# Kernel tuning notes

Measured on AMD Instinct MI355X. Metric: run time of the kernel, lower is better.

## Reference

```python
import jax, jax.numpy as jnp
import numpy as np
from jax import lax

LBDA = 0.5   # soft-min temperature from OTAM_cum_dist_v2 default
EPS = 0.01   # cos_sim epsilon


def otam_cum_dist(dists, lbda=LBDA):
    """Soft-DTW-style OTAM DP. dists: [nq, ns, L, S] -> [nq, ns].
    Faithful to OTAM_cum_dist_v2: pad last dim by (1,1) with zeros, then run the
    row-wise recurrence. Soft-min computed via stable logsumexp (same math as
    -lbda*log(sum exp(-x/lbda)))."""
    nq, ns, L, S = dists.shape
    d = jnp.pad(dists, ((0, 0), (0, 0), (0, 0), (1, 1)))  # [nq, ns, L, W], W=S+2
    W = S + 2
    # Row 0: cum[0, m] = cum[0, m-1] + d[0, m], cum[0, 0] = 0
    row0 = jnp.concatenate(
        [jnp.zeros((nq, ns, 1), d.dtype), jnp.cumsum(d[:, :, 0, 1:], axis=-1)], axis=-1)
    if L == 1:
        return row0[..., -1]

    m_idx = jnp.arange(1, W)
    include_up = (m_idx == 1) | (m_idx == W - 1)  # only first/last cols use cum[l-1, m]
    INF = jnp.asarray(jnp.inf, d.dtype)

    def row_step(prev_row, d_row):
        # prev_row, d_row: [nq, ns, W]
        xs = (
            jnp.moveaxis(d_row[:, :, 1:], -1, 0),        # d[l, m],       [W-1, nq, ns]
            jnp.moveaxis(prev_row[:, :, :-1], -1, 0),    # cum[l-1, m-1]
            jnp.moveaxis(prev_row[:, :, 1:], -1, 0),     # cum[l-1, m]
            include_up,
        )

        def col_step(cur_left, x):
            d_m, p_diag, p_up, inc = x
            up = jnp.where(inc, p_up, INF)               # masked term -> exp(-inf)=0
            terms = jnp.stack([p_diag, cur_left, up])    # [3, nq, ns]
            new = d_m - lbda * jax.nn.logsumexp(-terms / lbda, axis=0)
            return new, new

        _, cols = lax.scan(col_step, jnp.zeros((nq, ns), d.dtype), xs)
        row = jnp.concatenate(
            [jnp.zeros((nq, ns, 1), d.dtype), jnp.moveaxis(cols, 0, -1)], axis=-1)
        return row, None

    d_rows = jnp.moveaxis(d[:, :, 1:, :], 2, 0)          # [L-1, nq, ns, W]
    final_row, _ = lax.scan(row_step, row0, d_rows)
    return final_row[..., -1]


def reference(support_features, query_features):
    """OTAM meta-logits (cum_dist_g = -otam_distance) of DSN_TEMPORAL.
    support_features: [n_classes, L, D] class prototypes; query_features: [nq, L, D]."""
    nq, Lq, D = query_features.shape
    ns, Ls, _ = support_features.shape
    q = query_features.reshape(nq * Lq, D)
    s = support_features.reshape(ns * Ls, D)
    # cos_sim with epsilon in denominator (faithful to cos_sim())
    num = q @ s.T
    den = (jnp.linalg.norm(q, axis=-1)[:, None]
           * jnp.linalg.norm(s, axis=-1)[None, :] + EPS)
    frame_dists = 1.0 - num / den                         # [nq*L, ns*S]
    dists = frame_dists.reshape(nq, Lq, ns, Ls).transpose(0, 2, 1, 3)  # [nq, ns, L, S]
    cum = otam_cum_dist(dists) + otam_cum_dist(dists.transpose(0, 1, 3, 2))
    return -cum                                           # meta_logits [nq, ns]


def setup_inputs() -> dict:
    key = jax.random.key(0)
    k1, k2 = jax.random.split(key)
    return {
        "support_features": jax.random.normal(k1, (64, 8, 576), dtype=jnp.float32),
        "query_features": jax.random.normal(k2, (2048, 8, 576), dtype=jnp.float32),
    }
```

## Files before the change

### kernel.cpp

```cpp
#include <hip/hip_runtime.h>

#define D_K 576
#define NSLAB 18
#define LBDA_INV 2.0f
#define HALF_LBDA 0.5f
#define EPS 0.01f
#define DSTRIDE 136
#define DT_STRIDE 72
#define POOL_USHORTS 17920

typedef __attribute__((ext_vector_type(8))) short short8;
typedef __attribute__((ext_vector_type(4))) float f32x4;

__device__ inline unsigned cvt_pk_bf16(float lo, float hi) {
    unsigned r;
    asm("v_cvt_pk_bf16_f32 %0, %1, %2" : "=v"(r) : "v"(lo), "v"(hi));
    return r;
}

__device__ inline float softmin2(float a, float b) {
    float mn = fminf(a, b), mx = fmaxf(a, b);
    return mn - HALF_LBDA * __logf(1.f + __expf(LBDA_INV * (mn - mx)));
}
__device__ inline float softmin3(float a, float b, float c) {
    float mn = fminf(fminf(a, b), c);
    float mx = fmaxf(fmaxf(a, b), c);
    float md = __builtin_amdgcn_fmed3f(a, b, c);
    float s = 1.f + __expf(LBDA_INV * (mn - md)) + __expf(LBDA_INV * (mn - mx));
    return mn - HALF_LBDA * __logf(s);
}

template <int STRIDE>
__device__ float otam_dp_rows(const unsigned short* base) {
    float x[8], prev[10], cur[10];
    auto load_row = [&](int l) {
        uint4 v = *(const uint4*)(base + l * STRIDE);
        x[0] = __uint_as_float(v.x << 16);
        x[1] = __uint_as_float(v.x & 0xFFFF0000u);
        x[2] = __uint_as_float(v.y << 16);
        x[3] = __uint_as_float(v.y & 0xFFFF0000u);
        x[4] = __uint_as_float(v.z << 16);
        x[5] = __uint_as_float(v.z & 0xFFFF0000u);
        x[6] = __uint_as_float(v.w << 16);
        x[7] = __uint_as_float(v.w & 0xFFFF0000u);
    };
    load_row(0);
    prev[0] = 0.f;
#pragma unroll
    for (int m = 1; m <= 8; ++m) prev[m] = prev[m - 1] + x[m - 1];
    prev[9] = prev[8];
#pragma unroll
    for (int l = 1; l < 8; ++l) {
        load_row(l);
        cur[0] = 0.f;
        cur[1] = x[0] + softmin3(prev[0], 0.f, prev[1]);
#pragma unroll
        for (int m = 2; m <= 8; ++m)
            cur[m] = x[m - 1] + softmin2(prev[m - 1], cur[m - 1]);
        cur[9] = softmin3(prev[8], cur[8], prev[9]);
#pragma unroll
        for (int m = 0; m < 10; ++m) prev[m] = cur[m];
    }
    return prev[9];
}

__global__ __launch_bounds__(256, 4) void fused_kernel(
        const float* __restrict__ sup, const float* __restrict__ qry,
        float* __restrict__ out) {
    __shared__ __align__(16) unsigned short pool[POOL_USHORTS];
    __shared__ float qn_l[64], sn_l[128];
    unsigned short* const Bs0 = pool;
    unsigned short* const Bs1 = pool + 4096;
    unsigned short* const Ds  = pool;
    unsigned short* const DsT = pool + 8704;

    const int t = threadIdx.x;
    const int b = blockIdx.x;
    const int xcd = b & 7, s2 = b >> 3;
    const int sblk = s2 >> 5;
    const int qh = xcd * 32 + (s2 & 31);

    const float* qsrc = qry + (size_t)qh * 64 * D_K;
    const float* ssrc = sup + (size_t)sblk * 128 * D_K;

    const int rr = t >> 3;
    const int cc = t & 7;
    const int c_in = cc >> 1, half = cc & 1;

    const int lane = t & 63;
    const int wave = t >> 6;
    const int wm = wave >> 1, wn = wave & 1;
    const int col16 = lane & 15, quad = lane >> 4;

    f32x4 acc[2][4];
#pragma unroll
    for (int i = 0; i < 2; ++i)
#pragma unroll
        for (int j = 0; j < 4; ++j) acc[i][j] = (f32x4){0.f, 0.f, 0.f, 0.f};

    int agoff[2];
#pragma unroll
    for (int mt = 0; mt < 2; ++mt)
        agoff[mt] = (wm * 32 + mt * 16 + col16) * D_K + quad * 8;

    int boff[4], woff[4];
#pragma unroll
    for (int nt = 0; nt < 4; ++nt) {
        int n = wn * 64 + nt * 16 + col16;
        boff[nt] = (quad * 128 + (n ^ (quad << 1))) * 8;
    }
#pragma unroll
    for (int j = 0; j < 4; ++j)
        woff[j] = (c_in * 128 + ((j * 32 + rr) ^ (c_in << 1))) * 8 + half * 4;

    float ssA[2] = {0.f, 0.f}, ssB[4] = {0.f, 0.f, 0.f, 0.f};
    float4 vb[4];

    auto stage_load = [&](int sl) {
        const int off = sl * 32 + cc * 4;
#pragma unroll
        for (int j = 0; j < 4; ++j)
            vb[j] = *(const float4*)(ssrc + (size_t)(j * 32 + rr) * D_K + off);
    };
    auto stage_write = [&](unsigned short* __restrict__ B) {
#pragma unroll
        for (int j = 0; j < 4; ++j) {
            ssB[j] += vb[j].x * vb[j].x + vb[j].y * vb[j].y +
                      vb[j].z * vb[j].z + vb[j].w * vb[j].w;
            uint2 u;
            u.x = cvt_pk_bf16(vb[j].x, vb[j].y);
            u.y = cvt_pk_bf16(vb[j].z, vb[j].w);
            *(uint2*)(&B[woff[j]]) = u;
        }
    };
    auto compute = [&](int sl, const unsigned short* __restrict__ B) {
        float4 a0[2], a1[2];
#pragma unroll
        for (int mt = 0; mt < 2; ++mt) {
            const float* ap = qsrc + agoff[mt] + sl * 32;
            a0[mt] = *(const float4*)(ap);
            a1[mt] = *(const float4*)(ap + 4);
        }
        short8 bq[4];
#pragma unroll
        for (int nt = 0; nt < 4; ++nt) bq[nt] = *(const short8*)(&B[boff[nt]]);
        short8 af[2];
#pragma unroll
        for (int mt = 0; mt < 2; ++mt) {
            ssA[mt] += a0[mt].x * a0[mt].x + a0[mt].y * a0[mt].y +
                       a0[mt].z * a0[mt].z + a0[mt].w * a0[mt].w +
                       a1[mt].x * a1[mt].x + a1[mt].y * a1[mt].y +
                       a1[mt].z * a1[mt].z + a1[mt].w * a1[mt].w;
            uint4 u;
            u.x = cvt_pk_bf16(a0[mt].x, a0[mt].y);
            u.y = cvt_pk_bf16(a0[mt].z, a0[mt].w);
            u.z = cvt_pk_bf16(a1[mt].x, a1[mt].y);
            u.w = cvt_pk_bf16(a1[mt].z, a1[mt].w);
            af[mt] = *(short8*)&u;
        }
#pragma unroll
        for (int mt = 0; mt < 2; ++mt)
#pragma unroll
            for (int nt = 0; nt < 4; ++nt)
                acc[mt][nt] = __builtin_amdgcn_mfma_f32_16x16x32_bf16(
                    af[mt], bq[nt], acc[mt][nt], 0, 0, 0);
    };

    stage_load(0);
    stage_write(Bs0);
    __syncthreads();

#pragma unroll 1
    for (int sp = 0; sp < 9; ++sp) {
        stage_load(2 * sp + 1);
        compute(2 * sp, Bs0);
        stage_write(Bs1);
        __syncthreads();
        if (sp < 8) stage_load(2 * sp + 2);
        compute(2 * sp + 1, Bs1);
        if (sp < 8) stage_write(Bs0);
        __syncthreads();
    }

#pragma unroll
    for (int mt = 0; mt < 2; ++mt) {
        float a = ssA[mt];
        a += __shfl_down(a, 32);
        a += __shfl_down(a, 16);
        if (wn == 0 && lane < 16) qn_l[wm * 32 + mt * 16 + lane] = sqrtf(a);
    }
#pragma unroll
    for (int j = 0; j < 4; ++j) {
        float s = ssB[j];
        s += __shfl_down(s, 4); s += __shfl_down(s, 2); s += __shfl_down(s, 1);
        if ((t & 7) == 0) sn_l[j * 32 + rr] = sqrtf(s);
    }
    __syncthreads();

#pragma unroll
    for (int mt = 0; mt < 2; ++mt) {
        const int m = wm * 32 + mt * 16 + quad * 4;
        float q0 = qn_l[m], q1 = qn_l[m + 1], q2 = qn_l[m + 2], q3 = qn_l[m + 3];
#pragma unroll
        for (int nt = 0; nt < 4; ++nt) {
            const int n = wn * 64 + nt * 16 + col16;
            float sv = sn_l[n];
            float d0 = 1.f - acc[mt][nt][0] * __builtin_amdgcn_rcpf(q0 * sv + EPS);
            float d1 = 1.f - acc[mt][nt][1] * __builtin_amdgcn_rcpf(q1 * sv + EPS);
            float d2 = 1.f - acc[mt][nt][2] * __builtin_amdgcn_rcpf(q2 * sv + EPS);
            float d3 = 1.f - acc[mt][nt][3] * __builtin_amdgcn_rcpf(q3 * sv + EPS);
            uint2 u;
            u.x = cvt_pk_bf16(d0, d1);
            u.y = cvt_pk_bf16(d2, d3);
            *(uint2*)(&DsT[n * DT_STRIDE + m]) = u;
            Ds[(m + 0) * DSTRIDE + n] = (unsigned short)(u.x);
            Ds[(m + 1) * DSTRIDE + n] = (unsigned short)(u.x >> 16);
            Ds[(m + 2) * DSTRIDE + n] = (unsigned short)(u.y);
            Ds[(m + 3) * DSTRIDE + n] = (unsigned short)(u.y >> 16);
        }
    }
    __syncthreads();

    const int p = t & 127, ql = p >> 4, sj = p & 15;
    float r;
    if (t < 128) {
        r = otam_dp_rows<DSTRIDE>(Ds + (ql * 8) * DSTRIDE + sj * 8);
    } else {
        r = otam_dp_rows<DT_STRIDE>(DsT + (sj * 8) * DT_STRIDE + ql * 8);
        sn_l[p] = r;
    }
    __syncthreads();
    if (t < 128) {
        int qg = qh * 8 + ql, sg = sblk * 16 + sj;
        out[qg * 64 + sg] = -(r + sn_l[p]);
    }
}

extern "C" void kernel_launch(void* const* d_in, const int* in_sizes, int n_in,
                              void* d_out, int out_size, void* d_ws, size_t ws_size,
                              hipStream_t stream) {
    const float* sup = (const float*)d_in[0];
    const float* qry = (const float*)d_in[1];
    float* out = (float*)d_out;
    (void)d_ws; (void)ws_size;
    fused_kernel<<<dim3(1024), dim3(256), 0, stream>>>(sup, qry, out);
}
```

Baseline: 127.1 us.

## Load support B fragments directly from global memory, dropping LDS staging

```diff
diff --git a/kernel.cpp b/kernel.cpp
--- a/kernel.cpp
+++ b/kernel.cpp
@@ -69,8 +69,6 @@
         float* __restrict__ out) {
     __shared__ __align__(16) unsigned short pool[POOL_USHORTS];
     __shared__ float qn_l[64], sn_l[128];
-    unsigned short* const Bs0 = pool;
-    unsigned short* const Bs1 = pool + 4096;
     unsigned short* const Ds  = pool;
     unsigned short* const DsT = pool + 8704;
 
@@ -83,10 +81,6 @@
     const float* qsrc = qry + (size_t)qh * 64 * D_K;
     const float* ssrc = sup + (size_t)sblk * 128 * D_K;
 
-    const int rr = t >> 3;
-    const int cc = t & 7;
-    const int c_in = cc >> 1, half = cc & 1;
-
     const int lane = t & 63;
     const int wave = t >> 6;
     const int wm = wave >> 1, wn = wave & 1;
@@ -98,52 +92,32 @@
 #pragma unroll
         for (int j = 0; j < 4; ++j) acc[i][j] = (f32x4){0.f, 0.f, 0.f, 0.f};
 
-    int agoff[2];
+    int agoff[2], bgoff[4];
 #pragma unroll
     for (int mt = 0; mt < 2; ++mt)
         agoff[mt] = (wm * 32 + mt * 16 + col16) * D_K + quad * 8;
-
-    int boff[4], woff[4];
-#pragma unroll
-    for (int nt = 0; nt < 4; ++nt) {
-        int n = wn * 64 + nt * 16 + col16;
-        boff[nt] = (quad * 128 + (n ^ (quad << 1))) * 8;
-    }
-#pragma unroll
-    for (int j = 0; j < 4; ++j)
-        woff[j] = (c_in * 128 + ((j * 32 + rr) ^ (c_in << 1))) * 8 + half * 4;
+#pragma unroll
+    for (int nt = 0; nt < 4; ++nt)
+        bgoff[nt] = (wn * 64 + nt * 16 + col16) * D_K + quad * 8;
 
     float ssA[2] = {0.f, 0.f}, ssB[4] = {0.f, 0.f, 0.f, 0.f};
-    float4 vb[4];
-
-    auto stage_load = [&](int sl) {
-        const int off = sl * 32 + cc * 4;
-#pragma unroll
-        for (int j = 0; j < 4; ++j)
-            vb[j] = *(const float4*)(ssrc + (size_t)(j * 32 + rr) * D_K + off);
-    };
-    auto stage_write = [&](unsigned short* __restrict__ B) {
-#pragma unroll
-        for (int j = 0; j < 4; ++j) {
-            ssB[j] += vb[j].x * vb[j].x + vb[j].y * vb[j].y +
-                      vb[j].z * vb[j].z + vb[j].w * vb[j].w;
-            uint2 u;
-            u.x = cvt_pk_bf16(vb[j].x, vb[j].y);
-            u.y = cvt_pk_bf16(vb[j].z, vb[j].w);
-            *(uint2*)(&B[woff[j]]) = u;
-        }
-    };
-    auto compute = [&](int sl, const unsigned short* __restrict__ B) {
-        float4 a0[2], a1[2];
+
+#pragma unroll 1
+    for (int sl = 0; sl < NSLAB; ++sl) {
+        const int ko = sl * 32;
+        float4 a0[2], a1[2], b0[4], b1[4];
 #pragma unroll
         for (int mt = 0; mt < 2; ++mt) {
-            const float* ap = qsrc + agoff[mt] + sl * 32;
+            const float* ap = qsrc + agoff[mt] + ko;
             a0[mt] = *(const float4*)(ap);
             a1[mt] = *(const float4*)(ap + 4);
         }
-        short8 bq[4];
-#pragma unroll
-        for (int nt = 0; nt < 4; ++nt) bq[nt] = *(const short8*)(&B[boff[nt]]);
+#pragma unroll
+        for (int nt = 0; nt < 4; ++nt) {
+            const float* bp = ssrc + bgoff[nt] + ko;
+            b0[nt] = *(const float4*)(bp);
+            b1[nt] = *(const float4*)(bp + 4);
+        }
         short8 af[2];
 #pragma unroll
         for (int mt = 0; mt < 2; ++mt) {
@@ -159,27 +133,22 @@
             af[mt] = *(short8*)&u;
         }
 #pragma unroll
-        for (int mt = 0; mt < 2; ++mt)
-#pragma unroll
-            for (int nt = 0; nt < 4; ++nt)
+        for (int nt = 0; nt < 4; ++nt) {
+            ssB[nt] += b0[nt].x * b0[nt].x + b0[nt].y * b0[nt].y +
+                       b0[nt].z * b0[nt].z + b0[nt].w * b0[nt].w +
+                       b1[nt].x * b1[nt].x + b1[nt].y * b1[nt].y +
+                       b1[nt].z * b1[nt].z + b1[nt].w * b1[nt].w;
+            uint4 u;
+            u.x = cvt_pk_bf16(b0[nt].x, b0[nt].y);
+            u.y = cvt_pk_bf16(b0[nt].z, b0[nt].w);
+            u.z = cvt_pk_bf16(b1[nt].x, b1[nt].y);
+            u.w = cvt_pk_bf16(b1[nt].z, b1[nt].w);
+            short8 bq = *(short8*)&u;
+#pragma unroll
+            for (int mt = 0; mt < 2; ++mt)
                 acc[mt][nt] = __builtin_amdgcn_mfma_f32_16x16x32_bf16(
-                    af[mt], bq[nt], acc[mt][nt], 0, 0, 0);
-    };
-
-    stage_load(0);
-    stage_write(Bs0);
-    __syncthreads();
-
-#pragma unroll 1
-    for (int sp = 0; sp < 9; ++sp) {
-        stage_load(2 * sp + 1);
-        compute(2 * sp, Bs0);
-        stage_write(Bs1);
-        __syncthreads();
-        if (sp < 8) stage_load(2 * sp + 2);
-        compute(2 * sp + 1, Bs1);
-        if (sp < 8) stage_write(Bs0);
-        __syncthreads();
+                    af[mt], bq, acc[mt][nt], 0, 0, 0);
+        }
     }
 
 #pragma unroll
@@ -190,10 +159,11 @@
         if (wn == 0 && lane < 16) qn_l[wm * 32 + mt * 16 + lane] = sqrtf(a);
     }
 #pragma unroll
-    for (int j = 0; j < 4; ++j) {
-        float s = ssB[j];
-        s += __shfl_down(s, 4); s += __shfl_down(s, 2); s += __shfl_down(s, 1);
-        if ((t & 7) == 0) sn_l[j * 32 + rr] = sqrtf(s);
+    for (int nt = 0; nt < 4; ++nt) {
+        float s = ssB[nt];
+        s += __shfl_down(s, 32);
+        s += __shfl_down(s, 16);
+        if (wm == 0 && lane < 16) sn_l[wn * 64 + nt * 16 + lane] = sqrtf(s);
     }
     __syncthreads();
 
```

Measured after the change: 193.1 us. 52.0% more time.
